# Performance work log

Measured on AMD Instinct MI355X. Metric: run time of the kernel, lower is better.

The kernel has to match this reference:

```python
import jax, jax.numpy as jnp
import numpy as np

B, S, C, H = 2, 2048, 2048, 16
Dh = C // H
ROPE_THETA = 10000.0


def _rope(t):
    # t: [B, S, H, Dh]; rotate-half RoPE over head_dim
    half = Dh // 2
    inv_freq = 1.0 / (ROPE_THETA ** (jnp.arange(0, half, dtype=jnp.float32) / half))
    ang = jnp.arange(S, dtype=jnp.float32)[:, None] * inv_freq[None, :]  # [S, half]
    cos = jnp.cos(ang)[None, :, None, :]  # [1,S,1,half]
    sin = jnp.sin(ang)[None, :, None, :]
    t1, t2 = t[..., :half], t[..., half:]
    return jnp.concatenate([t1 * cos - t2 * sin, t2 * cos + t1 * sin], axis=-1)


def setup_inputs() -> dict:
    key = jax.random.key(0)
    k1, k2, k3 = jax.random.split(key, 3)
    x = jax.random.normal(k1, (B, S, C), dtype=jnp.float32)
    Wqkv = jax.random.normal(k2, (C, 3 * C), dtype=jnp.float32) * (C ** -0.5)
    Wproj = jax.random.normal(k3, (C, C), dtype=jnp.float32) * (C ** -0.5)
    return {"x": x, "Wqkv": Wqkv, "Wproj": Wproj}


def reference(x, Wqkv, Wproj):
    batch, seq, hidden = x.shape
    qkv = x @ Wqkv  # [B,S,3C]
    # NOTE: torch code chunks as k, q, v (k first)
    k, q, v = jnp.split(qkv, 3, axis=-1)
    k = k.reshape(batch, seq, H, Dh)
    q = q.reshape(batch, seq, H, Dh)
    v = v.reshape(batch, seq, H, Dh)
    k = _rope(k)
    q = _rope(q)
    scale = Dh ** -0.5
    scores = jnp.einsum('bqhd,bkhd->bhqk', q, k) * scale  # [B,H,S,S]
    causal = jnp.tril(jnp.ones((seq, seq), dtype=bool))
    scores = jnp.where(causal[None, None], scores, jnp.finfo(scores.dtype).min)
    attn = jax.nn.softmax(scores, axis=-1)
    out = jnp.einsum('bhqk,bkhd->bqhd', attn, v).reshape(batch, seq, hidden)
    return out @ Wproj
```

## Files before the change

kernel.cpp:

```cpp
#include <hip/hip_runtime.h>
#include <hip/hip_bf16.h>

#define B_   2
#define S_   2048
#define C_   2048
#define H_   16
#define DH   128
#define C3   (3 * C_)

typedef __attribute__((ext_vector_type(8))) short short8;
typedef __attribute__((ext_vector_type(4))) float floatx4;

__device__ __forceinline__ void gload16(const void* g, void* l) {
  __builtin_amdgcn_global_load_lds(
      (const __attribute__((address_space(1))) unsigned int*)g,
      (__attribute__((address_space(3))) unsigned int*)l, 16, 0, 0);
}

__device__ __forceinline__ unsigned pk_bf16(float a, float b) {
  union { __hip_bfloat16 h; unsigned short u; } ua, ub;
  ua.h = __float2bfloat16(a); ub.h = __float2bfloat16(b);
  return (unsigned)ua.u | ((unsigned)ub.u << 16);
}

__device__ __forceinline__ float bf2f(short u) {
  union { unsigned u; float f; } t;
  t.u = ((unsigned)(unsigned short)u) << 16;
  return t.f;
}
__device__ __forceinline__ short f2bf(float f) {
  union { __hip_bfloat16 h; short s; } t;
  t.h = __float2bfloat16(f);
  return t.s;
}

__device__ __forceinline__ void transpose_cast_dev(
    const float* __restrict__ in, __hip_bfloat16* __restrict__ out,
    int R, int Cc, int c0, int r0, int tid, float (*tile)[33]) {
  int tx = tid & 31, ty = tid >> 5;
#pragma unroll
  for (int k = 0; k < 4; ++k)
    tile[ty + 8 * k][tx] = in[(size_t)(r0 + ty + 8 * k) * Cc + c0 + tx];
  __syncthreads();
#pragma unroll
  for (int k = 0; k < 4; ++k)
    out[(size_t)(c0 + ty + 8 * k) * R + r0 + tx] = __float2bfloat16(tile[tx][ty + 8 * k]);
}

__global__ __launch_bounds__(256) void pre_kernel(
    const float* __restrict__ x, __hip_bfloat16* __restrict__ xb,
    const float* __restrict__ Wqkv, __hip_bfloat16* __restrict__ WqkvT) {
  __shared__ float tile[32][33];
  const int bid = blockIdx.x, tid = threadIdx.x;
  if (bid < 8192) {
    int i = bid * 256 + tid;
    float4 v = ((const float4*)x)[i];
    union { __hip_bfloat16 b[4]; uint2 u; } t;
    t.b[0] = __float2bfloat16(v.x);
    t.b[1] = __float2bfloat16(v.y);
    t.b[2] = __float2bfloat16(v.z);
    t.b[3] = __float2bfloat16(v.w);
    ((uint2*)xb)[i] = t.u;
  } else {
    int tb = bid - 8192;
    int bx = tb % 192, by = tb / 192;
    transpose_cast_dev(Wqkv, WqkvT, 2048, 6144, bx * 32, by * 32, tid, tile);
  }
}

#define S_VMCNT2 do { asm volatile("s_waitcnt vmcnt(2)" ::: "memory"); \
                      __builtin_amdgcn_sched_barrier(0); } while (0)
#define S_LGKM0  do { asm volatile("s_waitcnt lgkmcnt(0)" ::: "memory"); \
                      __builtin_amdgcn_sched_barrier(0); } while (0)
#define S_BAR    do { __builtin_amdgcn_s_barrier(); \
                      __builtin_amdgcn_sched_barrier(0); } while (0)


#define RD_A4(dst, buf, mh, sl)                                                          \
  do {                                                                                   \
    const __hip_bfloat16* base_ =                                                        \
        lds + (buf) * 28672 + (wm * 128 + (mh) * 64 + lr) * 64 + ((sl) ? sw1 : sw0);     \
    _Pragma("unroll") for (int i_ = 0; i_ < 4; ++i_)                                     \
        dst[i_] = *(const short8*)(base_ + i_ * 1024);                                   \
  } while (0)

#define RD_B3(dst, buf, sl)                                                              \
  do {                                                                                   \
    const __hip_bfloat16* base_ =                                                        \
        lds + (buf) * 28672 + 16384 + (wn * 48 + lr) * 64 + ((sl) ? sw1 : sw0);          \
    _Pragma("unroll") for (int j_ = 0; j_ < 3; ++j_)                                     \
        dst[j_] = *(const short8*)(base_ + j_ * 1024);                                   \
  } while (0)

#define MFG(afp, bfp, mh)                                                                \
  do {                                                                                   \
    __builtin_amdgcn_s_setprio(1);                                                       \
    _Pragma("unroll") for (int i_ = 0; i_ < 4; ++i_)                                     \
    _Pragma("unroll") for (int j_ = 0; j_ < 3; ++j_)                                     \
        acc[(mh) * 4 + i_][j_] = __builtin_amdgcn_mfma_f32_16x16x32_bf16(                \
            afp[i_], bfp[j_], acc[(mh) * 4 + i_][j_], 0, 0, 0);                          \
    __builtin_amdgcn_s_setprio(0);                                                       \
  } while (0)

__global__ __launch_bounds__(512, 2) void gemm1_kernel(
    const __hip_bfloat16* __restrict__ A, const __hip_bfloat16* __restrict__ Bt,
    __hip_bfloat16* __restrict__ Cp) {
  const int K = 2048;
  __shared__ __hip_bfloat16 lds[2 * 28672];
  const int tid = threadIdx.x;
  const int lane = tid & 63, wv = tid >> 6;
  const int wm = wv >> 2, wn = wv & 3;
  const int lr = lane & 15, lq = lane >> 4;
  const int m0 = blockIdx.y * 256, n0 = blockIdx.x * 192;
  const int sw0 = (lq ^ (lr & 7)) << 3;
  const int sw1 = sw0 ^ 32;

  const __hip_bfloat16* Abase = A + (size_t)m0 * K;
  const __hip_bfloat16* Bbase = Bt + (size_t)n0 * K;

  auto stA = [&](int buf, int half, int kk) {
#pragma unroll
    for (int pp = 0; pp < 2; ++pp) {
      int p = half * 2 + pp;
      int idx = p * 512 + tid;
      int row = idx >> 3;
      int lc = (idx & 7) ^ (row & 7);
      gload16(Abase + (size_t)row * K + kk + lc * 8,
              (char*)lds + buf * 57344 + p * 8192 + wv * 1024);
    }
  };
  auto stB2 = [&](int buf, int kk) {
#pragma unroll
    for (int p = 0; p < 2; ++p) {
      int idx = p * 512 + tid;
      int row = idx >> 3;
      int lc = (idx & 7) ^ (row & 7);
      gload16(Bbase + (size_t)row * K + kk + lc * 8,
              (char*)lds + buf * 57344 + 32768 + p * 8192 + wv * 1024);
    }
  };
  auto stB1 = [&](int buf, int kk) {
    int idx = 2 * 512 + tid;
    int row = idx >> 3;
    int lc = (idx & 7) ^ (row & 7);
    gload16(Bbase + (size_t)row * K + kk + lc * 8,
            (char*)lds + buf * 57344 + 49152 + wv * 1024);
  };

  floatx4 acc[8][3] = {};
  short8 afA[4], afB[4], afC[4], afD[4], bfA[3], bfB[3];

  stA(0, 0, 0); stA(0, 1, 0); stB2(0, 0); stB1(0, 0);
  stA(1, 0, 64);

#pragma unroll 1
  for (int it = 0; it < 16; ++it) {
    const int t = 2 * it;
    const int kk1 = (t + 1) * 64;
    const int kk2 = (t + 2 < 32) ? (t + 2) * 64 : 0;
    const int kk3 = (t + 3 < 32) ? (t + 3) * 64 : 0;

    S_VMCNT2; S_BAR;
    RD_A4(afA, 0, 0, 0); RD_B3(bfA, 0, 0);
    stA(1, 1, kk1);
    S_LGKM0;
    MFG(afA, bfA, 0);
    S_BAR;
    RD_A4(afB, 0, 1, 0); RD_A4(afC, 0, 0, 1);
    stB2(1, kk1);
    S_LGKM0;
    MFG(afB, bfA, 1);
    S_BAR;
    RD_B3(bfB, 0, 1); RD_A4(afD, 0, 1, 1);
    stB1(1, kk1);
    S_LGKM0;
    MFG(afC, bfB, 0);
    S_BAR;
    stA(0, 0, kk2);
    MFG(afD, bfB, 1);
    S_BAR;

    S_VMCNT2; S_BAR;
    RD_A4(afA, 1, 0, 0); RD_B3(bfA, 1, 0);
    stA(0, 1, kk2);
    S_LGKM0;
    MFG(afA, bfA, 0);
    S_BAR;
    RD_A4(afB, 1, 1, 0); RD_A4(afC, 1, 0, 1);
    stB2(0, kk2);
    S_LGKM0;
    MFG(afB, bfA, 1);
    S_BAR;
    RD_B3(bfB, 1, 1); RD_A4(afD, 1, 1, 1);
    stB1(0, kk2);
    S_LGKM0;
    MFG(afC, bfB, 0);
    S_BAR;
    stA(1, 0, kk3);
    MFG(afD, bfB, 1);
    S_BAR;
  }

  asm volatile("s_waitcnt vmcnt(0)" ::: "memory");
  __builtin_amdgcn_sched_barrier(0);

#pragma unroll
  for (int i = 0; i < 8; ++i)
#pragma unroll
    for (int j = 0; j < 3; ++j)
#pragma unroll
      for (int r = 0; r < 4; ++r) {
        int row = m0 + wm * 128 + i * 16 + lq * 4 + r;
        int col = n0 + wn * 48 + j * 16 + lr;
        Cp[(size_t)row * 6144 + col] = __float2bfloat16(acc[i][j][r]);
      }
}

#define S_VMCNT6 do { asm volatile("s_waitcnt vmcnt(6)" ::: "memory"); \
                      __builtin_amdgcn_sched_barrier(0); } while (0)

template <int NCOLS, bool OUT_F32>
__global__ __launch_bounds__(512, 2) void gemm_dp_kernel(
    const __hip_bfloat16* __restrict__ A, const __hip_bfloat16* __restrict__ Bt,
    void* __restrict__ Cp) {
  const int K = 2048, NT = 32;
  __shared__ __hip_bfloat16 lds[3 * 24576];
  const int tid = threadIdx.x;
  const int lane = tid & 63, wv = tid >> 6;
  const int wm = wv >> 1, wn = wv & 1;
  const int lr = lane & 15, lq = lane >> 4;
  const int m0 = blockIdx.y * 256, n0 = blockIdx.x * 128;
  const int sw0 = (lq ^ (lr & 7)) << 3;
  const int sw1 = sw0 ^ 32;

  auto stageA = [&](int bw, int p, int kk) {
    int idx = p * 512 + tid;
    int row = idx >> 3;
    int lc = (idx & 7) ^ (row & 7);
    gload16(A + (size_t)(m0 + row) * K + kk + lc * 8,
            (char*)lds + (size_t)bw * 49152 + (size_t)(p * 512 + wv * 64) * 16);
  };
  auto stageB = [&](int bw, int p, int kk) {
    int idx = p * 512 + tid;
    int row = idx >> 3;
    int lc = (idx & 7) ^ (row & 7);
    gload16(Bt + (size_t)(n0 + row) * K + kk + lc * 8,
            (char*)lds + (size_t)bw * 49152 + 32768 + (size_t)(p * 512 + wv * 64) * 16);
  };

#pragma unroll
  for (int p = 0; p < 4; ++p) stageA(0, p, 0);
#pragma unroll
  for (int p = 0; p < 2; ++p) stageB(0, p, 0);
#pragma unroll
  for (int p = 0; p < 4; ++p) stageA(1, p, 64);
#pragma unroll
  for (int p = 0; p < 2; ++p) stageB(1, p, 64);

  floatx4 acc[4][4] = {};
  int br = 0, bw = 2;

#pragma unroll 1
  for (int t = 0; t < NT; ++t) {
    const int kk2 = (t + 2 < NT) ? (t + 2) * 64 : 0;

    S_VMCNT6;
    S_BAR;

    const __hip_bfloat16* Ab = lds + br * 24576 + (wm * 64 + lr) * 64;
    const __hip_bfloat16* Bb = lds + br * 24576 + 16384 + (wn * 64 + lr) * 64;

    short8 af0[4], bf0[4];
#pragma unroll
    for (int i = 0; i < 4; ++i) af0[i] = *(const short8*)(Ab + i * 1024 + sw0);
#pragma unroll
    for (int j = 0; j < 4; ++j) bf0[j] = *(const short8*)(Bb + j * 1024 + sw0);
    stageA(bw, 0, kk2); stageA(bw, 1, kk2); stageB(bw, 0, kk2);
    S_LGKM0;
    __builtin_amdgcn_s_setprio(1);
#pragma unroll
    for (int i = 0; i < 4; ++i)
#pragma unroll
      for (int j = 0; j < 4; ++j)
        acc[i][j] = __builtin_amdgcn_mfma_f32_16x16x32_bf16(af0[i], bf0[j], acc[i][j], 0, 0, 0);
    __builtin_amdgcn_s_setprio(0);

    short8 af1[4], bf1[4];
#pragma unroll
    for (int i = 0; i < 4; ++i) af1[i] = *(const short8*)(Ab + i * 1024 + sw1);
#pragma unroll
    for (int j = 0; j < 4; ++j) bf1[j] = *(const short8*)(Bb + j * 1024 + sw1);
    stageA(bw, 2, kk2); stageA(bw, 3, kk2); stageB(bw, 1, kk2);
    S_LGKM0;
    __builtin_amdgcn_s_setprio(1);
#pragma unroll
    for (int i = 0; i < 4; ++i)
#pragma unroll
      for (int j = 0; j < 4; ++j)
        acc[i][j] = __builtin_amdgcn_mfma_f32_16x16x32_bf16(af1[i], bf1[j], acc[i][j], 0, 0, 0);
    __builtin_amdgcn_s_setprio(0);

    br = (br == 2) ? 0 : br + 1;
    bw = (bw == 2) ? 0 : bw + 1;
  }

  asm volatile("s_waitcnt vmcnt(0)" ::: "memory");
  __builtin_amdgcn_sched_barrier(0);

#pragma unroll
  for (int i = 0; i < 4; ++i)
#pragma unroll
    for (int j = 0; j < 4; ++j)
#pragma unroll
      for (int r = 0; r < 4; ++r) {
        int row = m0 + wm * 64 + i * 16 + lq * 4 + r;
        int col = n0 + wn * 64 + j * 16 + lr;
        if (OUT_F32)
          ((float*)Cp)[(size_t)row * NCOLS + col] = acc[i][j][r];
        else
          ((__hip_bfloat16*)Cp)[(size_t)row * NCOLS + col] = __float2bfloat16(acc[i][j][r]);
      }
}

__global__ __launch_bounds__(256) void mid_kernel(
    __hip_bfloat16* __restrict__ qkv, __hip_bfloat16* __restrict__ vt,
    const float* __restrict__ Wproj, __hip_bfloat16* __restrict__ WprojT) {
  __shared__ char smem[18432];
  const int bid = blockIdx.x, tid = threadIdx.x;

  if (bid < 2048) {
    int i = bid * 256 + tid;
    int d8 = (i & 7) << 3;
    int h = (i >> 3) & 15;
    int row = i >> 7;
    int s = row & (S_ - 1);
    size_t base = (size_t)row * C3 + h * DH + d8;
    short8 k1 = *(const short8*)(qkv + base);
    short8 k2 = *(const short8*)(qkv + base + 64);
    short8 q1 = *(const short8*)(qkv + base + C_);
    short8 q2 = *(const short8*)(qkv + base + C_ + 64);
    short8 ko1, ko2, qo1, qo2;
    const float scale = 0.08838834764831845f * 1.4426950408889634f;
#pragma unroll
    for (int j = 0; j < 8; ++j) {
      float invf = exp2f((float)(d8 + j) * (-13.287712379549449f / 64.0f));
      float ang = (float)s * invf;
      float sn, c;
      __sincosf(ang, &sn, &c);
      float a = bf2f(k1[j]), b = bf2f(k2[j]);
      ko1[j] = f2bf(a * c - b * sn);
      ko2[j] = f2bf(b * c + a * sn);
      a = bf2f(q1[j]); b = bf2f(q2[j]);
      qo1[j] = f2bf((a * c - b * sn) * scale);
      qo2[j] = f2bf((b * c + a * sn) * scale);
    }
    *(short8*)(qkv + base) = ko1;
    *(short8*)(qkv + base + 64) = ko2;
    *(short8*)(qkv + base + C_) = qo1;
    *(short8*)(qkv + base + C_ + 64) = qo2;
  } else if (bid < 3072) {
    short* T = (short*)smem;
    const int t = (bid - 2048) & 31, bh = (bid - 2048) >> 5;
    const int b = bh >> 4, h = bh & 15;
    const size_t brow = (size_t)b * S_;
#pragma unroll
    for (int p = 0; p < 4; ++p) {
      int idx = p * 256 + tid;
      int row = idx >> 4, c8 = idx & 15;
      *(short8*)(T + row * 144 + c8 * 8) =
          *(const short8*)(qkv + (brow + t * 64 + row) * C3 + 2 * C_ + h * DH + c8 * 8);
    }
    __syncthreads();
#pragma unroll
    for (int p = 0; p < 4; ++p) {
      int L = p * 256 + tid;
      int d = L & 127, cs = L >> 7;
      short8 v;
#pragma unroll
      for (int j = 0; j < 8; ++j) v[j] = T[(cs * 8 + j) * 144 + d];
      *(short8*)(vt + ((size_t)bh * 32 + t) * 8192 + (size_t)L * 8) = v;
    }
  } else {
    int tb = bid - 3072;
    int bx = tb & 63, by = tb >> 6;
    transpose_cast_dev(Wproj, WprojT, 2048, 2048, bx * 32, by * 32, tid,
                       (float(*)[33])smem);
  }
}

__global__ __launch_bounds__(256, 2) void attn_kernel(
    const __hip_bfloat16* __restrict__ qkv,
    const __hip_bfloat16* __restrict__ vt_tiles,
    __hip_bfloat16* __restrict__ outp) {
  __shared__ __hip_bfloat16 Ks[64 * 128];
  __shared__ __hip_bfloat16 Vt[64 * 128];
  __shared__ __hip_bfloat16 Ps[4 * 32 * 72];

  const int tid = threadIdx.x, lane = tid & 63, wv = tid >> 6;
  const int lr = lane & 15, lq = lane >> 4;
  const int n = blockIdx.y * 16 + blockIdx.x;
  const int half = n >> 8, rr = n & 255;
  const int bh = rr >> 3, p = rr & 7;
  const int qt = half ? p : 15 - p;
  const int b = bh >> 4, h = bh & 15;
  const int q0 = qt * 128;
  const int q0w = q0 + wv * 32;
  const size_t brow = (size_t)b * S_;
  const int nkt = 2 * qt + 2;

  short8 qf[2][4];
#pragma unroll
  for (int rt = 0; rt < 2; ++rt)
#pragma unroll
    for (int ks = 0; ks < 4; ++ks)
      qf[rt][ks] = *(const short8*)(qkv + (brow + q0w + rt * 16 + lr) * C3 + C_ + h * DH + ks * 32 + lq * 8);

  short8 kreg[4], vreg[4];
  auto issue = [&](int kti) {
    if (kti >= nkt) kti = nkt - 1;
    const int kb = kti * 64;
#pragma unroll
    for (int pp = 0; pp < 4; ++pp) {
      int L = pp * 256 + tid;
      int srow = L >> 4;
      int ck = (L & 15) ^ (srow & 15);
      kreg[pp] = *(const short8*)(qkv + (brow + kb + srow) * C3 + h * DH + ck * 8);
      vreg[pp] = *(const short8*)(vt_tiles + ((size_t)bh * 32 + kti) * 8192 + (size_t)L * 8);
    }
  };
  auto commit = [&]() {
#pragma unroll
    for (int pp = 0; pp < 4; ++pp) {
      *(short8*)(Ks + (size_t)(pp * 256 + tid) * 8) = kreg[pp];
      *(short8*)(Vt + (size_t)(pp * 256 + tid) * 8) = vreg[pp];
    }
  };

  floatx4 of[2][8] = {};
  float l_run[2] = {0.0f, 0.0f};

  const int wrow_last = q0w + 31;

  issue(0);
  commit();
  __syncthreads();

  for (int kt = 0; kt < nkt; ++kt) {
    const int kb = kt * 64;
    issue(kt + 1);

    if (kb <= wrow_last) {
      floatx4 st[2][4] = {};
#pragma unroll
      for (int ks = 0; ks < 4; ++ks) {
        short8 kfr[4];
#pragma unroll
        for (int t4 = 0; t4 < 4; ++t4)
          kfr[t4] = *(const short8*)(Ks + ((t4 * 16 + lr) * 16 + ((ks * 4 + lq) ^ lr)) * 8);
#pragma unroll
        for (int rt = 0; rt < 2; ++rt)
#pragma unroll
          for (int t4 = 0; t4 < 4; ++t4)
            st[rt][t4] = __builtin_amdgcn_mfma_f32_16x16x32_bf16(kfr[t4], qf[rt][ks], st[rt][t4], 0, 0, 0);
      }

      if (kb + 63 > q0w) {
#pragma unroll
        for (int rt = 0; rt < 2; ++rt)
#pragma unroll
          for (int t4 = 0; t4 < 4; ++t4)
#pragma unroll
            for (int r = 0; r < 4; ++r) {
              int s = kb + t4 * 16 + lq * 4 + r;
              if (s > q0w + rt * 16 + lr) st[rt][t4][r] = -1e30f;
            }
      }

#pragma unroll
      for (int rt = 0; rt < 2; ++rt) {
        float rs = 0.0f;
#pragma unroll
        for (int t4 = 0; t4 < 4; ++t4)
#pragma unroll
          for (int r = 0; r < 4; ++r) {
            float pv = exp2f(st[rt][t4][r]);
            st[rt][t4][r] = pv;
            rs += pv;
          }
        rs += __shfl_xor(rs, 16);
        rs += __shfl_xor(rs, 32);
        l_run[rt] += rs;
      }

#pragma unroll
      for (int rt = 0; rt < 2; ++rt)
#pragma unroll
        for (int t4 = 0; t4 < 4; ++t4) {
          unsigned* pdst = (unsigned*)(Ps + (wv * 32 + rt * 16 + lr) * 72 + t4 * 16 + lq * 4);
          pdst[0] = pk_bf16(st[rt][t4][0], st[rt][t4][1]);
          pdst[1] = pk_bf16(st[rt][t4][2], st[rt][t4][3]);
        }

#pragma unroll
      for (int ks = 0; ks < 2; ++ks) {
        short8 pa[2];
#pragma unroll
        for (int rt = 0; rt < 2; ++rt)
          pa[rt] = *(const short8*)(Ps + (wv * 32 + rt * 16 + lr) * 72 + ks * 32 + lq * 8);
#pragma unroll
        for (int dt = 0; dt < 8; ++dt) {
          short8 vb = *(const short8*)(Vt + ((ks * 4 + lq) * 128 + dt * 16 + lr) * 8);
#pragma unroll
          for (int rt = 0; rt < 2; ++rt)
            of[rt][dt] = __builtin_amdgcn_mfma_f32_16x16x32_bf16(pa[rt], vb, of[rt][dt], 0, 0, 0);
        }
      }
    }

    __syncthreads();
    commit();
    __syncthreads();
  }

#pragma unroll
  for (int rt = 0; rt < 2; ++rt) {
    float linv = 1.0f / l_run[rt];
    floatx4 lv;
#pragma unroll
    for (int r = 0; r < 4; ++r) lv[r] = __shfl(linv, lq * 4 + r);
#pragma unroll
    for (int dt = 0; dt < 8; ++dt)
#pragma unroll
      for (int r = 0; r < 4; ++r)
        outp[(brow + q0w + rt * 16 + lq * 4 + r) * C_ + h * DH + dt * 16 + lr] =
            __float2bfloat16(of[rt][dt][r] * lv[r]);
  }
}

extern "C" void kernel_launch(void* const* d_in, const int* in_sizes, int n_in,
                              void* d_out, int out_size, void* d_ws, size_t ws_size,
                              hipStream_t stream) {
  const float* x = (const float*)d_in[0];
  const float* Wqkv = (const float*)d_in[1];
  const float* Wproj = (const float*)d_in[2];

  __hip_bfloat16* xb = (__hip_bfloat16*)d_ws;
  __hip_bfloat16* WqkvT = xb + (size_t)4096 * 2048;
  __hip_bfloat16* qkvb = WqkvT + (size_t)6144 * 2048;
  __hip_bfloat16* WprojT = WqkvT;
  __hip_bfloat16* vt_tiles = WqkvT + (size_t)2048 * 2048;
  __hip_bfloat16* attnb = xb;

  pre_kernel<<<8192 + 12288, 256, 0, stream>>>(x, xb, Wqkv, WqkvT);

  gemm1_kernel<<<dim3(6144 / 192, 4096 / 256), 512, 0, stream>>>(xb, WqkvT, qkvb);

  mid_kernel<<<2048 + 1024 + 4096, 256, 0, stream>>>(qkvb, vt_tiles, Wproj, WprojT);

  attn_kernel<<<dim3(16, 32), 256, 0, stream>>>(qkvb, vt_tiles, attnb);

  gemm_dp_kernel<2048, true><<<dim3(2048 / 128, 4096 / 256), 512, 0, stream>>>(
      attnb, WprojT, (float*)d_out);
}
```

Before: 342.5 us.

## Double-buffer K/V in LDS, shuffle P in registers, vectorize transpose-cast

The attention kernel now keeps two LDS buffers for the K and V tiles. The next tile is committed into the other buffer, which removes one __syncthreads per key tile. The P matrix no longer goes through an LDS staging buffer: the bf16 probabilities are rearranged into MFMA A-operand layout with lane shuffles. The transpose-cast helper also switches to float4 loads and 8-byte packed bf16 stores. In exchange, LDS use grows to 64KB per block, which may limit occupancy at 2 blocks per CU, and the shuffle path adds many ds_bpermute operations.

```diff
diff --git a/kernel.cpp b/kernel.cpp
--- a/kernel.cpp
+++ b/kernel.cpp
@@ -37,14 +37,18 @@
 __device__ __forceinline__ void transpose_cast_dev(
     const float* __restrict__ in, __hip_bfloat16* __restrict__ out,
     int R, int Cc, int c0, int r0, int tid, float (*tile)[33]) {
-  int tx = tid & 31, ty = tid >> 5;
-#pragma unroll
-  for (int k = 0; k < 4; ++k)
-    tile[ty + 8 * k][tx] = in[(size_t)(r0 + ty + 8 * k) * Cc + c0 + tx];
+  int row = tid >> 3, col4 = tid & 7;
+  float4 v = *(const float4*)&in[(size_t)(r0 + row) * Cc + c0 + col4 * 4];
+  tile[row][col4 * 4 + 0] = v.x;
+  tile[row][col4 * 4 + 1] = v.y;
+  tile[row][col4 * 4 + 2] = v.z;
+  tile[row][col4 * 4 + 3] = v.w;
   __syncthreads();
-#pragma unroll
-  for (int k = 0; k < 4; ++k)
-    out[(size_t)(c0 + ty + 8 * k) * R + r0 + tx] = __float2bfloat16(tile[tx][ty + 8 * k]);
+  int c = tid >> 3, r4 = tid & 7;
+  union { __hip_bfloat16 b[4]; uint2 u; } t;
+#pragma unroll
+  for (int e = 0; e < 4; ++e) t.b[e] = __float2bfloat16(tile[r4 * 4 + e][c]);
+  *(uint2*)&out[(size_t)(c0 + c) * R + r0 + r4 * 4] = t.u;
 }
 
 __global__ __launch_bounds__(256) void pre_kernel(
@@ -392,9 +396,8 @@
     const __hip_bfloat16* __restrict__ qkv,
     const __hip_bfloat16* __restrict__ vt_tiles,
     __hip_bfloat16* __restrict__ outp) {
-  __shared__ __hip_bfloat16 Ks[64 * 128];
-  __shared__ __hip_bfloat16 Vt[64 * 128];
-  __shared__ __hip_bfloat16 Ps[4 * 32 * 72];
+  __shared__ __hip_bfloat16 Ks[2][8192];
+  __shared__ __hip_bfloat16 Vt[2][8192];
 
   const int tid = threadIdx.x, lane = tid & 63, wv = tid >> 6;
   const int lr = lane & 15, lq = lane >> 4;
@@ -403,10 +406,10 @@
   const int bh = rr >> 3, p = rr & 7;
   const int qt = half ? p : 15 - p;
   const int b = bh >> 4, h = bh & 15;
-  const int q0 = qt * 128;
-  const int q0w = q0 + wv * 32;
+  const int q0w = qt * 128 + wv * 32;
   const size_t brow = (size_t)b * S_;
   const int nkt = 2 * qt + 2;
+  const int wrow_last = q0w + 31;
 
   short8 qf[2][4];
 #pragma unroll
@@ -428,25 +431,24 @@
       vreg[pp] = *(const short8*)(vt_tiles + ((size_t)bh * 32 + kti) * 8192 + (size_t)L * 8);
     }
   };
-  auto commit = [&]() {
+  auto commit = [&](int buf) {
 #pragma unroll
     for (int pp = 0; pp < 4; ++pp) {
-      *(short8*)(Ks + (size_t)(pp * 256 + tid) * 8) = kreg[pp];
-      *(short8*)(Vt + (size_t)(pp * 256 + tid) * 8) = vreg[pp];
+      *(short8*)(Ks[buf] + (size_t)(pp * 256 + tid) * 8) = kreg[pp];
+      *(short8*)(Vt[buf] + (size_t)(pp * 256 + tid) * 8) = vreg[pp];
     }
   };
 
   floatx4 of[2][8] = {};
   float l_run[2] = {0.0f, 0.0f};
 
-  const int wrow_last = q0w + 31;
-
   issue(0);
-  commit();
+  commit(0);
   __syncthreads();
 
   for (int kt = 0; kt < nkt; ++kt) {
     const int kb = kt * 64;
+    const int buf = kt & 1;
     issue(kt + 1);
 
     if (kb <= wrow_last) {
@@ -456,7 +458,7 @@
         short8 kfr[4];
 #pragma unroll
         for (int t4 = 0; t4 < 4; ++t4)
-          kfr[t4] = *(const short8*)(Ks + ((t4 * 16 + lr) * 16 + ((ks * 4 + lq) ^ lr)) * 8);
+          kfr[t4] = *(const short8*)(Ks[buf] + ((t4 * 16 + lr) * 16 + ((ks * 4 + lq) ^ lr)) * 8);
 #pragma unroll
         for (int rt = 0; rt < 2; ++rt)
 #pragma unroll
@@ -492,24 +494,37 @@
         l_run[rt] += rs;
       }
 
+      unsigned pkL[2][4], pkH[2][4];
 #pragma unroll
       for (int rt = 0; rt < 2; ++rt)
 #pragma unroll
         for (int t4 = 0; t4 < 4; ++t4) {
-          unsigned* pdst = (unsigned*)(Ps + (wv * 32 + rt * 16 + lr) * 72 + t4 * 16 + lq * 4);
-          pdst[0] = pk_bf16(st[rt][t4][0], st[rt][t4][1]);
-          pdst[1] = pk_bf16(st[rt][t4][2], st[rt][t4][3]);
+          pkL[rt][t4] = pk_bf16(st[rt][t4][0], st[rt][t4][1]);
+          pkH[rt][t4] = pk_bf16(st[rt][t4][2], st[rt][t4][3]);
         }
+      const int s0 = (lq & 1) * 32 + lr;
+      const int s1 = s0 + 16;
+      const bool hi = (lq >> 1) != 0;
 
 #pragma unroll
       for (int ks = 0; ks < 2; ++ks) {
         short8 pa[2];
 #pragma unroll
-        for (int rt = 0; rt < 2; ++rt)
-          pa[rt] = *(const short8*)(Ps + (wv * 32 + rt * 16 + lr) * 72 + ks * 32 + lq * 8);
+        for (int rt = 0; rt < 2; ++rt) {
+          unsigned aL0 = __shfl(pkL[rt][2 * ks], s0), aL1 = __shfl(pkL[rt][2 * ks + 1], s0);
+          unsigned aH0 = __shfl(pkH[rt][2 * ks], s0), aH1 = __shfl(pkH[rt][2 * ks + 1], s0);
+          unsigned bL0 = __shfl(pkL[rt][2 * ks], s1), bL1 = __shfl(pkL[rt][2 * ks + 1], s1);
+          unsigned bH0 = __shfl(pkH[rt][2 * ks], s1), bH1 = __shfl(pkH[rt][2 * ks + 1], s1);
+          union { unsigned u[4]; short8 v; } pu;
+          pu.u[0] = hi ? aL1 : aL0;
+          pu.u[1] = hi ? aH1 : aH0;
+          pu.u[2] = hi ? bL1 : bL0;
+          pu.u[3] = hi ? bH1 : bH0;
+          pa[rt] = pu.v;
+        }
 #pragma unroll
         for (int dt = 0; dt < 8; ++dt) {
-          short8 vb = *(const short8*)(Vt + ((ks * 4 + lq) * 128 + dt * 16 + lr) * 8);
+          short8 vb = *(const short8*)(Vt[buf] + ((ks * 4 + lq) * 128 + dt * 16 + lr) * 8);
 #pragma unroll
           for (int rt = 0; rt < 2; ++rt)
             of[rt][dt] = __builtin_amdgcn_mfma_f32_16x16x32_bf16(pa[rt], vb, of[rt][dt], 0, 0, 0);
@@ -517,8 +532,7 @@
       }
     }
 
-    __syncthreads();
-    commit();
+    commit(buf ^ 1);
     __syncthreads();
   }
 
```

Result: no change. 345.4 us (+0.8%).
